# Performance work log

Measured on AMD Instinct MI355X. Metric: run time of the kernel, lower is better.

Reference implementation:

```python
import jax, jax.numpy as jnp
import numpy as np

EPS = 1e-7  # K.epsilon()
ROUTINGS = 3


def squash(v, axis=-1):
    s2 = jnp.sum(jnp.square(v), axis=axis, keepdims=True)
    scale = s2 / (1.0 + s2) / jnp.sqrt(s2 + EPS)
    return scale * v


def setup_inputs() -> dict:
    key = jax.random.key(0)
    kx, kw = jax.random.split(key)
    B, In, Din, Nc, Dc = 64, 2048, 16, 32, 32
    x = jax.random.normal(kx, (B, In, Din), dtype=jnp.float32)
    W = jax.random.normal(kw, (Nc, In, Dc, Din), dtype=jnp.float32) * 0.05
    return {"x": x, "W": W}


def reference(x, W):
    # x: [B, In, Din]; W: [Nc, In, Dc, Din]
    # Prediction vectors u_hat[b,i,j,d] = sum_k W[j,i,d,k] * x[b,i,k]
    # (the original tf.scan over batch + batch_dot computes exactly this,
    #  serialized; here it is a single batched einsum)
    hat = jnp.einsum('bik,jidk->bijd', x, W)  # [B, In, Nc, Dc]
    b = jnp.zeros(hat.shape[:3], dtype=hat.dtype)  # routing logits [B, In, Nc]
    v = None
    for i in range(ROUTINGS):
        c = jax.nn.softmax(b, axis=2)                 # over output capsules Nc
        s = jnp.einsum('bij,bijd->bjd', c, hat)       # weighted sum over In
        v = squash(s, axis=-1)                        # [B, Nc, Dc]
        if i < ROUTINGS - 1:
            b = b + jnp.einsum('bijd,bjd->bij', hat, v)  # agreement update
    return v
```

## Files before the change

kernel.cpp:

```cpp
#include <hip/hip_runtime.h>
#include <math.h>


#define B_TOT   64
#define IN_CAPS 2048
#define DIN     16
#define NC      32
#define DC      32
#define JD      (NC * DC)
#define B_CHUNK 4
#define I_CHUNK 16
#define N_IG    (IN_CAPS / I_CHUNK)
#define N_BG    (B_TOT / B_CHUNK)
#define EPS_SQ  1e-7f

#define WT_CHUNKS ((size_t)IN_CAPS * 4096)

#define LDS_BARRIER() do {                                  \
    asm volatile("" ::: "memory");                          \
    asm volatile("s_waitcnt lgkmcnt(0)");                   \
    __builtin_amdgcn_s_barrier();                           \
    __builtin_amdgcn_sched_barrier(0);                      \
} while (0)

__global__ __launch_bounds__(256) void transpose_W(const float* __restrict__ W,
                                                   float* __restrict__ Wt)
{
    __shared__ float4 tile[4096];
    const int i = blockIdx.x;
    const int t = threadIdx.x;
    const float4* Wf = (const float4*)W;
    float4 v[16];
#pragma unroll
    for (int q = 0; q < 16; ++q) {
        const int c  = t + 256 * q;
        const int jj = c >> 7, off = c & 127;
        v[q] = Wf[((size_t)jj * IN_CAPS + i) * 128 + off];
    }
#pragma unroll
    for (int q = 0; q < 16; ++q) {
        const int c = t + 256 * q;
        tile[c ^ ((c >> 4) & 7)] = v[q];
    }
    __syncthreads();
    float4* Wo = (float4*)Wt + (size_t)i * 4096;
    const int j = t >> 3, dq = t & 7;
#pragma unroll
    for (int k4 = 0; k4 < 4; ++k4)
#pragma unroll
        for (int r = 0; r < 4; ++r) {
            const int cg = j * 128 + dq * 16 + r * 4 + k4;
            Wo[(k4 * 4 + r) * 256 + t] = tile[cg ^ dq];
        }
}

template <int TRANS>
__device__ __forceinline__ void wload(float4 (&w)[4], const float4* __restrict__ base,
                                      int il, int k4) {
    if (TRANS) {
        const float4* p = base + (size_t)il * 4096 + k4 * 1024;
        w[0] = p[0];
        w[1] = p[256];
        w[2] = p[512];
        w[3] = p[768];
    } else {
        const float4* p = base + (size_t)il * 128 + k4;
        w[0] = p[0];
        w[1] = p[4];
        w[2] = p[8];
        w[3] = p[12];
    }
}

template <bool ACCUM>
__device__ __forceinline__ void qcomp(const float4 (&w)[4],
                                      const float* __restrict__ xi,
                                      int k4, float (*__restrict__ dst)[4])
{
#pragma unroll
    for (int b = 0; b < B_CHUNK; ++b) {
        const float* xb = xi + (size_t)b * (IN_CAPS * DIN) + k4 * 4;
        const float x0 = xb[0], x1 = xb[1], x2 = xb[2], x3 = xb[3];
#pragma unroll
        for (int r = 0; r < 4; ++r) {
            const float s = w[r].x * x0 + w[r].y * x1 + w[r].z * x2 + w[r].w * x3;
            if (ACCUM) dst[b][r] += s;
            else       dst[b][r] = s;
        }
    }
}

template <int PHASE, int ATOMIC, int TRANS>
__launch_bounds__(256, 2)
__global__ void caps_pass(const float* __restrict__ x,
                          const float* __restrict__ Wp,
                          const float* __restrict__ vsum,
                          float* __restrict__ P)
{
    __shared__ float c_s[PHASE ? 2 : 1][B_CHUNK][NC];

    const int t    = threadIdx.x;
    const int j    = t >> 3;
    const int dq   = t & 7;
    const int doff = dq * 4;
    const int jd0  = j * DC + doff;

    const int r   = blockIdx.x;
    const int xcd = r & 7;
    const int s   = r >> 3;
    const int bg  = s & 15;
    const int ig  = (s >> 4) * 8 + xcd;
    const int b0  = bg * B_CHUNK;
    const int i0  = ig * I_CHUNK;

    const float4* base = TRANS
        ? (const float4*)Wp + (size_t)i0 * 4096 + t
        : (const float4*)Wp + ((size_t)j * IN_CAPS + i0) * 128 + doff * 4;

    float4 wE[4], wO[4];
    wload<TRANS>(wE, base, 0, 0);

    float acc[B_CHUNK][4];
#pragma unroll
    for (int b = 0; b < B_CHUNK; ++b)
#pragma unroll
        for (int dd = 0; dd < 4; ++dd) acc[b][dd] = 0.f;

    float h[B_CHUNK][4];
    int buf = 0;

#pragma unroll 1
    for (int il = 0; il < I_CHUNK; ++il) {
        const float* xi = x + ((size_t)b0 * IN_CAPS + (i0 + il)) * DIN;
        float (*dst)[4] = PHASE ? h : acc;

        wload<TRANS>(wO, base, il, 1);
        if (PHASE == 0) qcomp<true >(wE, xi, 0, acc);
        else            qcomp<false>(wE, xi, 0, h);
        wload<TRANS>(wE, base, il, 2);
        qcomp<true>(wO, xi, 1, dst);
        wload<TRANS>(wO, base, il, 3);
        qcomp<true>(wE, xi, 2, dst);
        if (il + 1 < I_CHUNK) wload<TRANS>(wE, base, il + 1, 0);
        qcomp<true>(wO, xi, 3, dst);

        if (PHASE == 1) {
            float lp[B_CHUNK];
#pragma unroll
            for (int b = 0; b < B_CHUNK; ++b) {
                const float4 vv =
                    *(const float4*)&vsum[(size_t)(b0 + b) * JD + jd0];
                lp[b] = h[b][0]*vv.x + h[b][1]*vv.y + h[b][2]*vv.z + h[b][3]*vv.w;
                lp[b] += __shfl_xor(lp[b], 1, 8);
                lp[b] += __shfl_xor(lp[b], 2, 8);
                lp[b] += __shfl_xor(lp[b], 4, 8);
            }
            if (dq == 0) {
#pragma unroll
                for (int b = 0; b < B_CHUNK; ++b) c_s[buf][b][j] = lp[b];
            }
            LDS_BARRIER();

            if (t < 128) {
                const int tb = t >> 5, tj = t & 31;
                const float l = c_s[buf][tb][tj];
                float m = l;
                m = fmaxf(m, __shfl_xor(m, 1, 32));
                m = fmaxf(m, __shfl_xor(m, 2, 32));
                m = fmaxf(m, __shfl_xor(m, 4, 32));
                m = fmaxf(m, __shfl_xor(m, 8, 32));
                m = fmaxf(m, __shfl_xor(m, 16, 32));
                const float e = __expf(l - m);
                float ss = e;
                ss += __shfl_xor(ss, 1, 32);
                ss += __shfl_xor(ss, 2, 32);
                ss += __shfl_xor(ss, 4, 32);
                ss += __shfl_xor(ss, 8, 32);
                ss += __shfl_xor(ss, 16, 32);
                c_s[buf][tb][tj] = e / ss;
            }
            LDS_BARRIER();

#pragma unroll
            for (int b = 0; b < B_CHUNK; ++b) {
                const float c = c_s[buf][b][j];
                acc[b][0] += c * h[b][0];
                acc[b][1] += c * h[b][1];
                acc[b][2] += c * h[b][2];
                acc[b][3] += c * h[b][3];
            }
            buf ^= 1;
        }
    }

    const float scale = (PHASE == 0) ? (1.f / NC) : 1.f;
    if (ATOMIC) {
#pragma unroll
        for (int b = 0; b < B_CHUNK; ++b) {
            float* dstp = &P[(size_t)(b0 + b) * JD + jd0];
            atomicAdd(dstp + 0, acc[b][0] * scale);
            atomicAdd(dstp + 1, acc[b][1] * scale);
            atomicAdd(dstp + 2, acc[b][2] * scale);
            atomicAdd(dstp + 3, acc[b][3] * scale);
        }
    } else {
        float* dstp = P + ((size_t)ig * B_TOT + b0) * JD + jd0;
#pragma unroll
        for (int b = 0; b < B_CHUNK; ++b) {
            *(float4*)(dstp + (size_t)b * JD) =
                make_float4(acc[b][0] * scale, acc[b][1] * scale,
                            acc[b][2] * scale, acc[b][3] * scale);
        }
    }
}

__global__ __launch_bounds__(256) void reduce_squash(
    const float* __restrict__ Pf, int nparts,
    float* __restrict__ VSUMf, float* __restrict__ OUTf, int mode)
{
    __shared__ float4 sl[4][64];
    const float4* P4 = (const float4*)Pf;
    const int t = threadIdx.x, i64 = t & 63, slice = t >> 6;
    const int idx = blockIdx.x * 64 + i64;
    float4 v = make_float4(0.f, 0.f, 0.f, 0.f);
    for (int ig = slice; ig < nparts; ig += 4) {
        const float4 p = P4[(size_t)ig * (B_TOT * JD / 4) + idx];
        v.x += p.x; v.y += p.y; v.z += p.z; v.w += p.w;
    }
    sl[slice][i64] = v;
    __syncthreads();
    if (t < 64) {
        const float4 a = sl[0][t], b = sl[1][t], c = sl[2][t], d = sl[3][t];
        v.x = a.x + b.x + c.x + d.x;
        v.y = a.y + b.y + c.y + d.y;
        v.z = a.z + b.z + c.z + d.z;
        v.w = a.w + b.w + c.w + d.w;
        float s2 = v.x*v.x + v.y*v.y + v.z*v.z + v.w*v.w;
        s2 += __shfl_xor(s2, 1, 8);
        s2 += __shfl_xor(s2, 2, 8);
        s2 += __shfl_xor(s2, 4, 8);
        const float sc = s2 / (1.f + s2) * rsqrtf(s2 + EPS_SQ);
        const int gidx = blockIdx.x * 64 + t;
        float4 o = make_float4(v.x * sc, v.y * sc, v.z * sc, v.w * sc);
        float4* VSUM = (float4*)VSUMf;
        float4* OUT  = (float4*)OUTf;
        if (mode == 0) {
            VSUM[gidx] = o;
        } else if (mode == 1) {
            float4 u = VSUM[gidx];
            u.x += o.x; u.y += o.y; u.z += o.z; u.w += o.w;
            VSUM[gidx] = u;
        } else {
            OUT[gidx] = o;
        }
    }
}

extern "C" void kernel_launch(void* const* d_in, const int* in_sizes, int n_in,
                              void* d_out, int out_size, void* d_ws, size_t ws_size,
                              hipStream_t stream)
{
    const float* x = (const float*)d_in[0];
    const float* W = (const float*)d_in[1];
    float* out = (float*)d_out;

    const dim3 grid(N_IG * N_BG);
    const dim3 blk(256);
    const dim3 rgrid(B_TOT * JD / 4 / 64);

    const size_t P_elems  = (size_t)N_IG * B_TOT * JD;
    const size_t vs_elems = (size_t)B_TOT * JD;
    const size_t need_p   = (P_elems + vs_elems) * sizeof(float);
    const size_t need_t   = (WT_CHUNKS * 4 + P_elems + vs_elems) * sizeof(float);

    if (ws_size >= need_t) {
        float* Wt   = (float*)d_ws;
        float* P    = Wt + WT_CHUNKS * 4;
        float* VSUM = P + P_elems;
        transpose_W<<<dim3(IN_CAPS), blk, 0, stream>>>(W, Wt);
        caps_pass<0, 0, 1><<<grid, blk, 0, stream>>>(x, Wt, nullptr, P);
        reduce_squash<<<rgrid, blk, 0, stream>>>(P, N_IG, VSUM, out, 0);
        caps_pass<1, 0, 1><<<grid, blk, 0, stream>>>(x, Wt, VSUM, P);
        reduce_squash<<<rgrid, blk, 0, stream>>>(P, N_IG, VSUM, out, 1);
        caps_pass<1, 0, 1><<<grid, blk, 0, stream>>>(x, Wt, VSUM, P);
        reduce_squash<<<rgrid, blk, 0, stream>>>(P, N_IG, VSUM, out, 2);
    } else if (ws_size >= need_p) {
        float* P    = (float*)d_ws;
        float* VSUM = P + P_elems;
        caps_pass<0, 0, 0><<<grid, blk, 0, stream>>>(x, W, nullptr, P);
        reduce_squash<<<rgrid, blk, 0, stream>>>(P, N_IG, VSUM, out, 0);
        caps_pass<1, 0, 0><<<grid, blk, 0, stream>>>(x, W, VSUM, P);
        reduce_squash<<<rgrid, blk, 0, stream>>>(P, N_IG, VSUM, out, 1);
        caps_pass<1, 0, 0><<<grid, blk, 0, stream>>>(x, W, VSUM, P);
        reduce_squash<<<rgrid, blk, 0, stream>>>(P, N_IG, VSUM, out, 2);
    } else {
        float* S    = (float*)d_ws;
        float* VSUM = S + vs_elems;
        const size_t sbytes = vs_elems * sizeof(float);
        hipMemsetAsync(S, 0, sbytes, stream);
        caps_pass<0, 1, 0><<<grid, blk, 0, stream>>>(x, W, nullptr, S);
        reduce_squash<<<rgrid, blk, 0, stream>>>(S, 1, VSUM, out, 0);
        hipMemsetAsync(S, 0, sbytes, stream);
        caps_pass<1, 1, 0><<<grid, blk, 0, stream>>>(x, W, VSUM, S);
        reduce_squash<<<rgrid, blk, 0, stream>>>(S, 1, VSUM, out, 1);
        hipMemsetAsync(S, 0, sbytes, stream);
        caps_pass<1, 1, 0><<<grid, blk, 0, stream>>>(x, W, VSUM, S);
        reduce_squash<<<rgrid, blk, 0, stream>>>(S, 1, VSUM, out, 2);
    }
}
```

Before: 597.0 us.

## Deepen W prefetch, hoist vsum loads, drop LDS transpose, widen reduce slices

The main caps pass now keeps four W register buffers, prefetching two quarters ahead instead of one, to better hide global load latency. The vsum loads move out of the per-input-capsule loop into registers. transpose_W drops the LDS tile and writes directly from per-thread register gathers. reduce_squash splits the partial-sum reduction across 8 slices of 32 elements, using twice as many blocks, to expose more memory parallelism. The extra register buffers raise register pressure and may reduce occupancy.

```diff
diff --git a/kernel.cpp b/kernel.cpp
--- a/kernel.cpp
+++ b/kernel.cpp
@@ -26,32 +26,21 @@
 __global__ __launch_bounds__(256) void transpose_W(const float* __restrict__ W,
                                                    float* __restrict__ Wt)
 {
-    __shared__ float4 tile[4096];
     const int i = blockIdx.x;
     const int t = threadIdx.x;
+    const int j = t >> 3, dq = t & 7;
     const float4* Wf = (const float4*)W;
+    float4* Wo = (float4*)Wt + (size_t)i * 4096;
+    const float4* src = Wf + ((size_t)j * IN_CAPS + i) * 128 + dq * 16;
     float4 v[16];
 #pragma unroll
-    for (int q = 0; q < 16; ++q) {
-        const int c  = t + 256 * q;
-        const int jj = c >> 7, off = c & 127;
-        v[q] = Wf[((size_t)jj * IN_CAPS + i) * 128 + off];
-    }
-#pragma unroll
-    for (int q = 0; q < 16; ++q) {
-        const int c = t + 256 * q;
-        tile[c ^ ((c >> 4) & 7)] = v[q];
-    }
-    __syncthreads();
-    float4* Wo = (float4*)Wt + (size_t)i * 4096;
-    const int j = t >> 3, dq = t & 7;
-#pragma unroll
     for (int k4 = 0; k4 < 4; ++k4)
 #pragma unroll
-        for (int r = 0; r < 4; ++r) {
-            const int cg = j * 128 + dq * 16 + r * 4 + k4;
-            Wo[(k4 * 4 + r) * 256 + t] = tile[cg ^ dq];
-        }
+        for (int r = 0; r < 4; ++r)
+            v[k4 * 4 + r] = src[r * 4 + k4];
+#pragma unroll
+    for (int q = 0; q < 16; ++q)
+        Wo[q * 256 + t] = v[q];
 }
 
 template <int TRANS>
@@ -117,8 +106,16 @@
         ? (const float4*)Wp + (size_t)i0 * 4096 + t
         : (const float4*)Wp + ((size_t)j * IN_CAPS + i0) * 128 + doff * 4;
 
-    float4 wE[4], wO[4];
-    wload<TRANS>(wE, base, 0, 0);
+    float4 vv[B_CHUNK];
+    if (PHASE) {
+#pragma unroll
+        for (int b = 0; b < B_CHUNK; ++b)
+            vv[b] = *(const float4*)&vsum[(size_t)(b0 + b) * JD + jd0];
+    }
+
+    float4 w0[4], w1[4], w2[4], w3[4];
+    wload<TRANS>(w0, base, 0, 0);
+    wload<TRANS>(w1, base, 0, 1);
 
     float acc[B_CHUNK][4];
 #pragma unroll
@@ -134,23 +131,22 @@
         const float* xi = x + ((size_t)b0 * IN_CAPS + (i0 + il)) * DIN;
         float (*dst)[4] = PHASE ? h : acc;
 
-        wload<TRANS>(wO, base, il, 1);
-        if (PHASE == 0) qcomp<true >(wE, xi, 0, acc);
-        else            qcomp<false>(wE, xi, 0, h);
-        wload<TRANS>(wE, base, il, 2);
-        qcomp<true>(wO, xi, 1, dst);
-        wload<TRANS>(wO, base, il, 3);
-        qcomp<true>(wE, xi, 2, dst);
-        if (il + 1 < I_CHUNK) wload<TRANS>(wE, base, il + 1, 0);
-        qcomp<true>(wO, xi, 3, dst);
+        wload<TRANS>(w2, base, il, 2);
+        if (PHASE == 0) qcomp<true >(w0, xi, 0, acc);
+        else            qcomp<false>(w0, xi, 0, h);
+        wload<TRANS>(w3, base, il, 3);
+        qcomp<true>(w1, xi, 1, dst);
+        if (il + 1 < I_CHUNK) wload<TRANS>(w0, base, il + 1, 0);
+        qcomp<true>(w2, xi, 2, dst);
+        if (il + 1 < I_CHUNK) wload<TRANS>(w1, base, il + 1, 1);
+        qcomp<true>(w3, xi, 3, dst);
 
         if (PHASE == 1) {
             float lp[B_CHUNK];
 #pragma unroll
             for (int b = 0; b < B_CHUNK; ++b) {
-                const float4 vv =
-                    *(const float4*)&vsum[(size_t)(b0 + b) * JD + jd0];
-                lp[b] = h[b][0]*vv.x + h[b][1]*vv.y + h[b][2]*vv.z + h[b][3]*vv.w;
+                lp[b] = h[b][0]*vv[b].x + h[b][1]*vv[b].y
+                      + h[b][2]*vv[b].z + h[b][3]*vv[b].w;
                 lp[b] += __shfl_xor(lp[b], 1, 8);
                 lp[b] += __shfl_xor(lp[b], 2, 8);
                 lp[b] += __shfl_xor(lp[b], 4, 8);
@@ -218,29 +214,31 @@
     const float* __restrict__ Pf, int nparts,
     float* __restrict__ VSUMf, float* __restrict__ OUTf, int mode)
 {
-    __shared__ float4 sl[4][64];
+    __shared__ float4 sl[8][32];
     const float4* P4 = (const float4*)Pf;
-    const int t = threadIdx.x, i64 = t & 63, slice = t >> 6;
-    const int idx = blockIdx.x * 64 + i64;
+    const int t = threadIdx.x, i32 = t & 31, slice = t >> 5;
+    const int idx = blockIdx.x * 32 + i32;
     float4 v = make_float4(0.f, 0.f, 0.f, 0.f);
-    for (int ig = slice; ig < nparts; ig += 4) {
+#pragma unroll 4
+    for (int ig = slice; ig < nparts; ig += 8) {
         const float4 p = P4[(size_t)ig * (B_TOT * JD / 4) + idx];
         v.x += p.x; v.y += p.y; v.z += p.z; v.w += p.w;
     }
-    sl[slice][i64] = v;
+    sl[slice][i32] = v;
     __syncthreads();
-    if (t < 64) {
-        const float4 a = sl[0][t], b = sl[1][t], c = sl[2][t], d = sl[3][t];
-        v.x = a.x + b.x + c.x + d.x;
-        v.y = a.y + b.y + c.y + d.y;
-        v.z = a.z + b.z + c.z + d.z;
-        v.w = a.w + b.w + c.w + d.w;
+    if (t < 32) {
+        v = sl[0][t];
+#pragma unroll
+        for (int k = 1; k < 8; ++k) {
+            const float4 p = sl[k][t];
+            v.x += p.x; v.y += p.y; v.z += p.z; v.w += p.w;
+        }
         float s2 = v.x*v.x + v.y*v.y + v.z*v.z + v.w*v.w;
         s2 += __shfl_xor(s2, 1, 8);
         s2 += __shfl_xor(s2, 2, 8);
         s2 += __shfl_xor(s2, 4, 8);
         const float sc = s2 / (1.f + s2) * rsqrtf(s2 + EPS_SQ);
-        const int gidx = blockIdx.x * 64 + t;
+        const int gidx = blockIdx.x * 32 + t;
         float4 o = make_float4(v.x * sc, v.y * sc, v.z * sc, v.w * sc);
         float4* VSUM = (float4*)VSUMf;
         float4* OUT  = (float4*)OUTf;
@@ -266,7 +264,7 @@
 
     const dim3 grid(N_IG * N_BG);
     const dim3 blk(256);
-    const dim3 rgrid(B_TOT * JD / 4 / 64);
+    const dim3 rgrid(B_TOT * JD / 4 / 32);
 
     const size_t P_elems  = (size_t)N_IG * B_TOT * JD;
     const size_t vs_elems = (size_t)B_TOT * JD;
```

Measured after the change: 626.4 us. 4.9% more time.
